# Performance work log

Hardware: AMD Instinct MI355X
Metric: run time of the kernel (lower is better)

Reference implementation:

```python
import jax, jax.numpy as jnp
import numpy as np

DIM_VAL = 128
DIM_ATTN = 64

def setup_inputs() -> dict:
    key = jax.random.key(0)
    k_x, k_q, k_k, k_v = jax.random.split(key, 4)
    B, S = 4, 4096
    x = jax.random.normal(k_x, (B, S, DIM_VAL), dtype=jnp.float32)
    # nn.Linear(in, out, bias=False): weight shape [out, in]; y = x @ W^T
    Wq = jax.random.normal(k_q, (DIM_ATTN, DIM_VAL), dtype=jnp.float32) / np.sqrt(DIM_VAL)
    Wk = jax.random.normal(k_k, (DIM_ATTN, DIM_VAL), dtype=jnp.float32) / np.sqrt(DIM_VAL)
    Wv = jax.random.normal(k_v, (DIM_VAL, DIM_VAL), dtype=jnp.float32) / np.sqrt(DIM_VAL)
    return {"x": x, "Wq": Wq, "Wk": Wk, "Wv": Wv}

def reference(x, Wq, Wk, Wv):
    # QKV projections (bias-free linear: x @ W^T)
    Q = jnp.einsum('bsd,ad->bsa', x, Wq)   # [B,S,dim_attn]
    K = jnp.einsum('bsd,ad->bsa', x, Wk)   # [B,S,dim_attn]
    V = jnp.einsum('bsd,vd->bsv', x, Wv)   # [B,S,dim_val]
    scale = 1.0 / jnp.sqrt(jnp.asarray(Q.shape[-1], dtype=Q.dtype))
    scores = jnp.einsum('bqa,bka->bqk', Q, K) * scale  # [B,S,S]
    a = jax.nn.softmax(scores, axis=-1)
    return jnp.einsum('bqk,bkv->bqv', a, V)  # [B,S,dim_val]
```

## Files before the change

kernel.cpp:

```cpp
#include <hip/hip_runtime.h>

typedef _Float16 half8 __attribute__((ext_vector_type(8)));
typedef _Float16 half4v __attribute__((ext_vector_type(4)));
typedef float   float4v __attribute__((ext_vector_type(4)));

#define S_LEN 4096
#define NBATCH 4
#define NCHUNK 4
#define WS_QH  32768
#define WS_KH  1081344
#define WS_VT  2129920
#define WS_L   4227072
#define OACC_BYTE_OFF 8519680ull
#define OACC_F4_PER_CHUNK (NBATCH * S_LEN * 128 / 4)
#define LACC_BYTE_OFF (OACC_BYTE_OFF + (unsigned long long)NCHUNK * NBATCH * S_LEN * 128 * 4)
#define WS_NEED_BYTES (LACC_BYTE_OFF + (unsigned long long)NCHUNK * NBATCH * S_LEN * 4)

static __device__ __forceinline__ half8 cvt8(float4v f0, float4v f1) {
    half8 h;
    h[0] = (_Float16)f0[0]; h[1] = (_Float16)f0[1];
    h[2] = (_Float16)f0[2]; h[3] = (_Float16)f0[3];
    h[4] = (_Float16)f1[0]; h[5] = (_Float16)f1[1];
    h[6] = (_Float16)f1[2]; h[7] = (_Float16)f1[3];
    return h;
}

static __device__ __forceinline__ void gload16(const _Float16* g, _Float16* l) {
    __builtin_amdgcn_global_load_lds(
        (const __attribute__((address_space(1))) void*)g,
        (__attribute__((address_space(3))) void*)l, 16, 0, 0);
}

__global__ __launch_bounds__(256) void zero_kernel(float4v* __restrict__ out4,
                                                   float4v* __restrict__ l4) {
    int i = blockIdx.x * 256 + threadIdx.x;
    out4[i] = (float4v){0.f, 0.f, 0.f, 0.f};
    if (i < 4096) l4[i] = (float4v){0.f, 0.f, 0.f, 0.f};
}

__global__ __launch_bounds__(256) void qkv_proj_kernel(const float* __restrict__ x,
                                                       const float* __restrict__ Wq,
                                                       const float* __restrict__ Wk,
                                                       const float* __restrict__ Wv,
                                                       _Float16* __restrict__ Qh,
                                                       _Float16* __restrict__ Kh,
                                                       _Float16* __restrict__ Vt) {
    const int t = threadIdx.x, blk = blockIdx.x;
    const int w = t >> 6, lane = t & 63, quad = lane >> 4, n16 = lane & 15;
    const float* xb = x + (size_t)blk * 16 * 128;

    half8 a[4];
#pragma unroll
    for (int c = 0; c < 4; ++c) {
        const float* xr = xb + n16 * 128 + c * 32 + quad * 8;
        a[c] = cvt8(*(const float4v*)xr, *(const float4v*)(xr + 4));
    }

    const float* Wsel = (w == 0) ? Wq : (w == 1) ? Wk : Wv;
    const int rowoff = (w >= 2) ? (w - 2) * 64 : 0;

    float4v acc[4];
#pragma unroll
    for (int nb = 0; nb < 4; ++nb) acc[nb] = (float4v){0.f, 0.f, 0.f, 0.f};

#pragma unroll
    for (int c = 0; c < 4; ++c)
#pragma unroll
        for (int nb = 0; nb < 4; ++nb) {
            const float* wr = Wsel + (size_t)(rowoff + nb * 16 + n16) * 128 + c * 32 + quad * 8;
            half8 bfr = cvt8(*(const float4v*)wr, *(const float4v*)(wr + 4));
            acc[nb] = __builtin_amdgcn_mfma_f32_16x16x32_f16(a[c], bfr, acc[nb], 0, 0, 0);
        }

    const int token0 = blk * 16 + quad * 4;
    if (w == 0) {
        for (int nb = 0; nb < 4; ++nb)
            for (int r = 0; r < 4; ++r)
                Qh[(size_t)(token0 + r) * 64 + nb * 16 + n16] = (_Float16)acc[nb][r];
    } else if (w == 1) {
        for (int nb = 0; nb < 4; ++nb)
            for (int r = 0; r < 4; ++r)
                Kh[(size_t)(token0 + r) * 64 + nb * 16 + n16] = (_Float16)acc[nb][r];
    } else {
        const int bb = token0 >> 12, s0 = token0 & 4095;
        const int kt = s0 >> 6, k0 = s0 & 63;
        const int grp = k0 >> 5, k32 = k0 & 31;
        const int g = k32 >> 4, q = (k32 >> 2) & 3;
        const int off = kt * 64 + grp * 32 + q * 8 + g * 4;
        for (int nb = 0; nb < 4; ++nb) {
            const int vc = (w - 2) * 64 + nb * 16 + n16;
            half4v h;
            h[0] = (_Float16)acc[nb][0]; h[1] = (_Float16)acc[nb][1];
            h[2] = (_Float16)acc[nb][2]; h[3] = (_Float16)acc[nb][3];
            *(half4v*)&Vt[((size_t)bb * 128 + vc) * S_LEN + off] = h;
        }
    }
}

#define KT 64
template <bool STAGED>
__global__ __launch_bounds__(256) void flash_kernel(const _Float16* __restrict__ Qh,
                                                    const _Float16* __restrict__ Kh,
                                                    const _Float16* __restrict__ Vt,
                                                    float* __restrict__ outp,
                                                    float* __restrict__ lp) {
    __shared__ _Float16 Ks[2][KT * 64];
    __shared__ _Float16 Vs[2][128 * 64];

    const int t = threadIdx.x;
    const int qt = blockIdx.x, chunk = blockIdx.y, b = blockIdx.z;
    const int w = t >> 6, lane = t & 63, quad = lane >> 4, n16 = lane & 15;
    const int swz = n16 & 7;

    const size_t qrowA = (size_t)b * S_LEN + qt * 128 + w * 16 + n16;
    const size_t qrowB = qrowA + 64;
    half8 aQ0A = *(const half8*)&Qh[qrowA * 64 + quad * 8];
    half8 aQ1A = *(const half8*)&Qh[qrowA * 64 + 32 + quad * 8];
    half8 aQ0B = *(const half8*)&Qh[qrowB * 64 + quad * 8];
    half8 aQ1B = *(const half8*)&Qh[qrowB * 64 + 32 + quad * 8];

    float4v OA[8], OB[8];
#pragma unroll
    for (int vb = 0; vb < 8; ++vb) {
        OA[vb] = (float4v){0.f, 0.f, 0.f, 0.f};
        OB[vb] = (float4v){0.f, 0.f, 0.f, 0.f};
    }
    float lsumA = 0.f, lsumB = 0.f;

    const _Float16* Kb = Kh + (size_t)b * S_LEN * 64;
    const _Float16* Vb = Vt + (size_t)b * 128 * S_LEN;

    const int kt0 = chunk * (S_LEN / KT / NCHUNK);
    const int kt1 = kt0 + (S_LEN / KT / NCHUNK);

#define STAGE(bb, ktv) do {                                                    \
        const _Float16* Ksrc = Kb + (size_t)(ktv) * KT * 64;                   \
        _Float16* Kdst = &Ks[bb][0];                                           \
        _Float16* Vdst = &Vs[bb][0];                                           \
        for (int i_ = 0; i_ < 2; ++i_) {                                       \
            int d_ = t + i_ * 256, row_ = d_ >> 3, ch_ = d_ & 7;               \
            gload16(Ksrc + row_ * 64 + ((ch_ ^ (row_ & 7)) << 3), Kdst + d_ * 8); \
        }                                                                      \
        for (int i_ = 0; i_ < 4; ++i_) {                                       \
            int d_ = t + i_ * 256, row_ = d_ >> 3, ch_ = d_ & 7;               \
            gload16(Vb + (size_t)row_ * S_LEN + (ktv) * KT + ((ch_ ^ (row_ & 7)) << 3), \
                    Vdst + d_ * 8);                                            \
        }                                                                      \
    } while (0)

    STAGE(0, kt0);
    asm volatile("s_waitcnt vmcnt(0)" ::: "memory");
    __builtin_amdgcn_s_barrier();

    int cur = 0;
    for (int kt = kt0; kt < kt1; ++kt) {
        if (kt + 1 < kt1) STAGE(cur ^ 1, kt + 1);

        const _Float16* Ksc = Ks[cur];
        const _Float16* Vsc = Vs[cur];

        half8 aP0A, aP1A, aP0B, aP1B;
        __builtin_amdgcn_s_setprio(1);
#pragma unroll
        for (int nb = 0; nb < 4; ++nb) {
            const int krow = (nb * 16 + n16) * 64;
            half8 bK0 = *(const half8*)&Ksc[krow + ((quad ^ swz) << 3)];
            half8 bK1 = *(const half8*)&Ksc[krow + (((4 + quad) ^ swz) << 3)];
            float4v scA = (float4v){0.f, 0.f, 0.f, 0.f};
            float4v scB = (float4v){0.f, 0.f, 0.f, 0.f};
            scA = __builtin_amdgcn_mfma_f32_16x16x32_f16(bK0, aQ0A, scA, 0, 0, 0);
            scA = __builtin_amdgcn_mfma_f32_16x16x32_f16(bK1, aQ1A, scA, 0, 0, 0);
            scB = __builtin_amdgcn_mfma_f32_16x16x32_f16(bK0, aQ0B, scB, 0, 0, 0);
            scB = __builtin_amdgcn_mfma_f32_16x16x32_f16(bK1, aQ1B, scB, 0, 0, 0);
#pragma unroll
            for (int r = 0; r < 4; ++r) {
                float pa = __builtin_amdgcn_exp2f(__builtin_fmaf(scA[r], 0.18033688f, -5.7707802f));
                lsumA += pa;
                float pb = __builtin_amdgcn_exp2f(__builtin_fmaf(scB[r], 0.18033688f, -5.7707802f));
                lsumB += pb;
                int slot = (nb & 1) * 4 + r;
                if (nb < 2) { aP0A[slot] = (_Float16)pa; aP0B[slot] = (_Float16)pb; }
                else        { aP1A[slot] = (_Float16)pa; aP1B[slot] = (_Float16)pb; }
            }
        }
        __builtin_amdgcn_s_setprio(0);

        __builtin_amdgcn_s_setprio(1);
#pragma unroll
        for (int vb = 0; vb < 8; ++vb) {
            const int vrow = (vb * 16 + n16) * 64;
            half8 bV0 = *(const half8*)&Vsc[vrow + ((quad ^ swz) << 3)];
            half8 bV1 = *(const half8*)&Vsc[vrow + (((4 + quad) ^ swz) << 3)];
            OA[vb] = __builtin_amdgcn_mfma_f32_16x16x32_f16(aP0A, bV0, OA[vb], 0, 0, 0);
            OA[vb] = __builtin_amdgcn_mfma_f32_16x16x32_f16(aP1A, bV1, OA[vb], 0, 0, 0);
            OB[vb] = __builtin_amdgcn_mfma_f32_16x16x32_f16(aP0B, bV0, OB[vb], 0, 0, 0);
            OB[vb] = __builtin_amdgcn_mfma_f32_16x16x32_f16(aP1B, bV1, OB[vb], 0, 0, 0);
        }
        __builtin_amdgcn_s_setprio(0);

        if (kt + 1 < kt1) {
            asm volatile("s_waitcnt vmcnt(0)" ::: "memory");
            __builtin_amdgcn_s_barrier();
            cur ^= 1;
        }
    }
#undef STAGE

    lsumA += __shfl_xor(lsumA, 16);
    lsumA += __shfl_xor(lsumA, 32);
    lsumB += __shfl_xor(lsumB, 16);
    lsumB += __shfl_xor(lsumB, 32);

    const int rowbaseA = qt * 128 + w * 16;
    const int rowbaseB = rowbaseA + 64;
    const int row0A = rowbaseA + quad * 4;
    const int row0B = rowbaseB + quad * 4;

    if (STAGED) {
        const size_t cb = (size_t)chunk * NBATCH + b;
        if (quad == 0) {
            lp[cb * S_LEN + rowbaseA + n16] = lsumA;
            lp[cb * S_LEN + rowbaseB + n16] = lsumB;
        }
        float* obA = outp + (cb * S_LEN + row0A) * 128;
        float* obB = outp + (cb * S_LEN + row0B) * 128;
#pragma unroll
        for (int vb = 0; vb < 8; ++vb)
#pragma unroll
            for (int r = 0; r < 4; ++r) {
                obA[(size_t)r * 128 + vb * 16 + n16] = OA[vb][r];
                obB[(size_t)r * 128 + vb * 16 + n16] = OB[vb][r];
            }
    } else {
        if (quad == 0) {
            unsafeAtomicAdd(&lp[b * S_LEN + rowbaseA + n16], lsumA);
            unsafeAtomicAdd(&lp[b * S_LEN + rowbaseB + n16], lsumB);
        }
        float* obA = outp + ((size_t)b * S_LEN + row0A) * 128;
        float* obB = outp + ((size_t)b * S_LEN + row0B) * 128;
#pragma unroll
        for (int vb = 0; vb < 8; ++vb)
#pragma unroll
            for (int r = 0; r < 4; ++r) {
                unsafeAtomicAdd(&obA[(size_t)r * 128 + vb * 16 + n16], OA[vb][r]);
                unsafeAtomicAdd(&obB[(size_t)r * 128 + vb * 16 + n16], OB[vb][r]);
            }
    }
}

__global__ __launch_bounds__(256) void norm_sum_kernel(const float4v* __restrict__ oacc4,
                                                       const float* __restrict__ lacc,
                                                       float4v* __restrict__ out4) {
    int i = blockIdx.x * 256 + threadIdx.x;
    int row = i >> 5;
    float l = 0.f;
#pragma unroll
    for (int c = 0; c < NCHUNK; ++c) l += lacc[c * (NBATCH * S_LEN) + row];
    float4v s = (float4v){0.f, 0.f, 0.f, 0.f};
#pragma unroll
    for (int c = 0; c < NCHUNK; ++c) {
        float4v p = oacc4[(size_t)c * OACC_F4_PER_CHUNK + i];
        s[0] += p[0]; s[1] += p[1]; s[2] += p[2]; s[3] += p[3];
    }
    float inv = 1.0f / l;
    s[0] *= inv; s[1] *= inv; s[2] *= inv; s[3] *= inv;
    out4[i] = s;
}

__global__ __launch_bounds__(256) void norm_kernel(float4v* __restrict__ out4,
                                                   const float* __restrict__ lbuf) {
    int i = blockIdx.x * 256 + threadIdx.x;
    float inv = 1.0f / lbuf[i >> 5];
    float4v v = out4[i];
    v[0] *= inv; v[1] *= inv; v[2] *= inv; v[3] *= inv;
    out4[i] = v;
}

extern "C" void kernel_launch(void* const* d_in, const int* in_sizes, int n_in,
                              void* d_out, int out_size, void* d_ws, size_t ws_size,
                              hipStream_t stream) {
    const float* x  = (const float*)d_in[0];
    const float* Wq = (const float*)d_in[1];
    const float* Wk = (const float*)d_in[2];
    const float* Wv = (const float*)d_in[3];
    float* out = (float*)d_out;

    _Float16* ws = (_Float16*)d_ws;
    _Float16* Qh  = ws + WS_QH;
    _Float16* Kh  = ws + WS_KH;
    _Float16* Vt  = ws + WS_VT;
    float*    lbuf = (float*)(ws + WS_L);

    qkv_proj_kernel<<<NBATCH * S_LEN / 16, 256, 0, stream>>>(x, Wq, Wk, Wv, Qh, Kh, Vt);

    if (ws_size >= (size_t)WS_NEED_BYTES) {
        float* oacc = (float*)((char*)d_ws + OACC_BYTE_OFF);
        float* lacc = (float*)((char*)d_ws + LACC_BYTE_OFF);
        flash_kernel<true><<<dim3(S_LEN / 128, NCHUNK, NBATCH), 256, 0, stream>>>(
            Qh, Kh, Vt, oacc, lacc);
        norm_sum_kernel<<<2048, 256, 0, stream>>>((const float4v*)oacc, lacc, (float4v*)out);
    } else {
        zero_kernel<<<2048, 256, 0, stream>>>((float4v*)out, (float4v*)lbuf);
        flash_kernel<false><<<dim3(S_LEN / 128, NCHUNK, NBATCH), 256, 0, stream>>>(
            Qh, Kh, Vt, out, lbuf);
        norm_kernel<<<2048, 256, 0, stream>>>((float4v*)out, lbuf);
    }
}
```

Baseline: 124.7 us.

## Pre-convert weights to fp16, stage x via LDS, and interleave softmax with PV MFMAs

Adds a small kernel that converts Wq/Wk/Wv to fp16 once into workspace. The projection kernel then reads fp16 weights and loads x through shared memory, instead of every block re-reading and re-converting fp32 weights. In the flash loop, the exp/pack step is split into two halves, each followed by its half of the PV MFMAs, so ALU and matrix work can overlap. The s_setprio hints are removed. This costs an extra kernel launch and more live score registers.

```diff
diff --git a/kernel.cpp b/kernel.cpp
--- a/kernel.cpp
+++ b/kernel.cpp
@@ -7,6 +7,7 @@
 #define S_LEN 4096
 #define NBATCH 4
 #define NCHUNK 4
+#define WS_W16 0
 #define WS_QH  32768
 #define WS_KH  1081344
 #define WS_VT  2129920
@@ -16,19 +17,23 @@
 #define LACC_BYTE_OFF (OACC_BYTE_OFF + (unsigned long long)NCHUNK * NBATCH * S_LEN * 128 * 4)
 #define WS_NEED_BYTES (LACC_BYTE_OFF + (unsigned long long)NCHUNK * NBATCH * S_LEN * 4)
 
-static __device__ __forceinline__ half8 cvt8(float4v f0, float4v f1) {
-    half8 h;
-    h[0] = (_Float16)f0[0]; h[1] = (_Float16)f0[1];
-    h[2] = (_Float16)f0[2]; h[3] = (_Float16)f0[3];
-    h[4] = (_Float16)f1[0]; h[5] = (_Float16)f1[1];
-    h[6] = (_Float16)f1[2]; h[7] = (_Float16)f1[3];
-    return h;
-}
-
 static __device__ __forceinline__ void gload16(const _Float16* g, _Float16* l) {
     __builtin_amdgcn_global_load_lds(
         (const __attribute__((address_space(1))) void*)g,
         (__attribute__((address_space(3))) void*)l, 16, 0, 0);
+}
+
+__global__ __launch_bounds__(256) void wcvt_kernel(const float* __restrict__ Wq,
+                                                   const float* __restrict__ Wk,
+                                                   const float* __restrict__ Wv,
+                                                   _Float16* __restrict__ w16) {
+    int i = blockIdx.x * 256 + threadIdx.x;
+    int row = i >> 7, col = i & 127;
+    float v;
+    if (row < 64)       v = Wq[row * 128 + col];
+    else if (row < 128) v = Wk[(row - 64) * 128 + col];
+    else                v = Wv[(row - 128) * 128 + col];
+    w16[i] = (_Float16)v;
 }
 
 __global__ __launch_bounds__(256) void zero_kernel(float4v* __restrict__ out4,
@@ -39,38 +44,42 @@
 }
 
 __global__ __launch_bounds__(256) void qkv_proj_kernel(const float* __restrict__ x,
-                                                       const float* __restrict__ Wq,
-                                                       const float* __restrict__ Wk,
-                                                       const float* __restrict__ Wv,
+                                                       const _Float16* __restrict__ w16,
                                                        _Float16* __restrict__ Qh,
                                                        _Float16* __restrict__ Kh,
                                                        _Float16* __restrict__ Vt) {
-    const int t = threadIdx.x, blk = blockIdx.x;
+    __shared__ _Float16 xs[16 * 136];
+    const int t = threadIdx.x;
+    const int blk = blockIdx.x;
+    const float* xb = x + (size_t)blk * 16 * 128;
+
+    for (int it = 0; it < 2; ++it) {
+        int i = t + it * 256;
+        int row = i >> 5, c4 = i & 31;
+        float4v f = ((const float4v*)xb)[i];
+        half4v h;
+        h[0] = (_Float16)f[0]; h[1] = (_Float16)f[1];
+        h[2] = (_Float16)f[2]; h[3] = (_Float16)f[3];
+        *(half4v*)&xs[row * 136 + c4 * 4] = h;
+    }
+    __syncthreads();
+
     const int w = t >> 6, lane = t & 63, quad = lane >> 4, n16 = lane & 15;
-    const float* xb = x + (size_t)blk * 16 * 128;
 
     half8 a[4];
-#pragma unroll
+    for (int c = 0; c < 4; ++c)
+        a[c] = *(const half8*)&xs[n16 * 136 + c * 32 + quad * 8];
+
+    float4v acc[4];
+    for (int nb = 0; nb < 4; ++nb) acc[nb] = (float4v){0.f, 0.f, 0.f, 0.f};
+
     for (int c = 0; c < 4; ++c) {
-        const float* xr = xb + n16 * 128 + c * 32 + quad * 8;
-        a[c] = cvt8(*(const float4v*)xr, *(const float4v*)(xr + 4));
-    }
-
-    const float* Wsel = (w == 0) ? Wq : (w == 1) ? Wk : Wv;
-    const int rowoff = (w >= 2) ? (w - 2) * 64 : 0;
-
-    float4v acc[4];
-#pragma unroll
-    for (int nb = 0; nb < 4; ++nb) acc[nb] = (float4v){0.f, 0.f, 0.f, 0.f};
-
-#pragma unroll
-    for (int c = 0; c < 4; ++c)
-#pragma unroll
         for (int nb = 0; nb < 4; ++nb) {
-            const float* wr = Wsel + (size_t)(rowoff + nb * 16 + n16) * 128 + c * 32 + quad * 8;
-            half8 bfr = cvt8(*(const float4v*)wr, *(const float4v*)(wr + 4));
+            int oc = w * 64 + nb * 16 + n16;
+            half8 bfr = *(const half8*)&w16[(size_t)oc * 128 + c * 32 + quad * 8];
             acc[nb] = __builtin_amdgcn_mfma_f32_16x16x32_f16(a[c], bfr, acc[nb], 0, 0, 0);
         }
+    }
 
     const int token0 = blk * 16 + quad * 4;
     if (w == 0) {
@@ -159,44 +168,61 @@
         const _Float16* Ksc = Ks[cur];
         const _Float16* Vsc = Vs[cur];
 
-        half8 aP0A, aP1A, aP0B, aP1B;
-        __builtin_amdgcn_s_setprio(1);
+        float4v scA[4], scB[4];
 #pragma unroll
         for (int nb = 0; nb < 4; ++nb) {
             const int krow = (nb * 16 + n16) * 64;
             half8 bK0 = *(const half8*)&Ksc[krow + ((quad ^ swz) << 3)];
             half8 bK1 = *(const half8*)&Ksc[krow + (((4 + quad) ^ swz) << 3)];
-            float4v scA = (float4v){0.f, 0.f, 0.f, 0.f};
-            float4v scB = (float4v){0.f, 0.f, 0.f, 0.f};
-            scA = __builtin_amdgcn_mfma_f32_16x16x32_f16(bK0, aQ0A, scA, 0, 0, 0);
-            scA = __builtin_amdgcn_mfma_f32_16x16x32_f16(bK1, aQ1A, scA, 0, 0, 0);
-            scB = __builtin_amdgcn_mfma_f32_16x16x32_f16(bK0, aQ0B, scB, 0, 0, 0);
-            scB = __builtin_amdgcn_mfma_f32_16x16x32_f16(bK1, aQ1B, scB, 0, 0, 0);
+            scA[nb] = (float4v){0.f, 0.f, 0.f, 0.f};
+            scB[nb] = (float4v){0.f, 0.f, 0.f, 0.f};
+            scA[nb] = __builtin_amdgcn_mfma_f32_16x16x32_f16(bK0, aQ0A, scA[nb], 0, 0, 0);
+            scA[nb] = __builtin_amdgcn_mfma_f32_16x16x32_f16(bK1, aQ1A, scA[nb], 0, 0, 0);
+            scB[nb] = __builtin_amdgcn_mfma_f32_16x16x32_f16(bK0, aQ0B, scB[nb], 0, 0, 0);
+            scB[nb] = __builtin_amdgcn_mfma_f32_16x16x32_f16(bK1, aQ1B, scB[nb], 0, 0, 0);
+        }
+
+        half8 aP0A, aP0B;
+#pragma unroll
+        for (int nb = 0; nb < 2; ++nb)
 #pragma unroll
             for (int r = 0; r < 4; ++r) {
-                float pa = __builtin_amdgcn_exp2f(__builtin_fmaf(scA[r], 0.18033688f, -5.7707802f));
+                float pa = __builtin_amdgcn_exp2f(__builtin_fmaf(scA[nb][r], 0.18033688f, -5.7707802f));
                 lsumA += pa;
-                float pb = __builtin_amdgcn_exp2f(__builtin_fmaf(scB[r], 0.18033688f, -5.7707802f));
+                float pb = __builtin_amdgcn_exp2f(__builtin_fmaf(scB[nb][r], 0.18033688f, -5.7707802f));
                 lsumB += pb;
-                int slot = (nb & 1) * 4 + r;
-                if (nb < 2) { aP0A[slot] = (_Float16)pa; aP0B[slot] = (_Float16)pb; }
-                else        { aP1A[slot] = (_Float16)pa; aP1B[slot] = (_Float16)pb; }
+                aP0A[nb * 4 + r] = (_Float16)pa;
+                aP0B[nb * 4 + r] = (_Float16)pb;
             }
-        }
-        __builtin_amdgcn_s_setprio(0);
-
-        __builtin_amdgcn_s_setprio(1);
+
 #pragma unroll
         for (int vb = 0; vb < 8; ++vb) {
             const int vrow = (vb * 16 + n16) * 64;
             half8 bV0 = *(const half8*)&Vsc[vrow + ((quad ^ swz) << 3)];
+            OA[vb] = __builtin_amdgcn_mfma_f32_16x16x32_f16(aP0A, bV0, OA[vb], 0, 0, 0);
+            OB[vb] = __builtin_amdgcn_mfma_f32_16x16x32_f16(aP0B, bV0, OB[vb], 0, 0, 0);
+        }
+
+        half8 aP1A, aP1B;
+#pragma unroll
+        for (int nb = 2; nb < 4; ++nb)
+#pragma unroll
+            for (int r = 0; r < 4; ++r) {
+                float pa = __builtin_amdgcn_exp2f(__builtin_fmaf(scA[nb][r], 0.18033688f, -5.7707802f));
+                lsumA += pa;
+                float pb = __builtin_amdgcn_exp2f(__builtin_fmaf(scB[nb][r], 0.18033688f, -5.7707802f));
+                lsumB += pb;
+                aP1A[(nb & 1) * 4 + r] = (_Float16)pa;
+                aP1B[(nb & 1) * 4 + r] = (_Float16)pb;
+            }
+
+#pragma unroll
+        for (int vb = 0; vb < 8; ++vb) {
+            const int vrow = (vb * 16 + n16) * 64;
             half8 bV1 = *(const half8*)&Vsc[vrow + (((4 + quad) ^ swz) << 3)];
-            OA[vb] = __builtin_amdgcn_mfma_f32_16x16x32_f16(aP0A, bV0, OA[vb], 0, 0, 0);
             OA[vb] = __builtin_amdgcn_mfma_f32_16x16x32_f16(aP1A, bV1, OA[vb], 0, 0, 0);
-            OB[vb] = __builtin_amdgcn_mfma_f32_16x16x32_f16(aP0B, bV0, OB[vb], 0, 0, 0);
             OB[vb] = __builtin_amdgcn_mfma_f32_16x16x32_f16(aP1B, bV1, OB[vb], 0, 0, 0);
         }
-        __builtin_amdgcn_s_setprio(0);
 
         if (kt + 1 < kt1) {
             asm volatile("s_waitcnt vmcnt(0)" ::: "memory");
@@ -286,12 +312,14 @@
     float* out = (float*)d_out;
 
     _Float16* ws = (_Float16*)d_ws;
+    _Float16* w16 = ws + WS_W16;
     _Float16* Qh  = ws + WS_QH;
     _Float16* Kh  = ws + WS_KH;
     _Float16* Vt  = ws + WS_VT;
     float*    lbuf = (float*)(ws + WS_L);
 
-    qkv_proj_kernel<<<NBATCH * S_LEN / 16, 256, 0, stream>>>(x, Wq, Wk, Wv, Qh, Kh, Vt);
+    wcvt_kernel<<<128, 256, 0, stream>>>(Wq, Wk, Wv, w16);
+    qkv_proj_kernel<<<NBATCH * S_LEN / 16, 256, 0, stream>>>(x, w16, Qh, Kh, Vt);
 
     if (ws_size >= (size_t)WS_NEED_BYTES) {
         float* oacc = (float*)((char*)d_ws + OACC_BYTE_OFF);
```

New measurement: 137.4 us. 10.1% more time.
